# Performance work log

Hardware: AMD Instinct MI355X
Metric: run time of the kernel (lower is better)

Reference implementation:

```python
import jax, jax.numpy as jnp
import numpy as np

EPS = 1e-7  # tf.keras.backend.epsilon()
DEGREE = 5
SCALE_BASE = 1.0
SCALE_LEGENDRE = 1.0


def legendre_basis(x, degree):
    # min/max normalization over the feature axis -> x_norm in [-1, 1]
    x_min = jnp.min(x, axis=-1, keepdims=True)
    x_max = jnp.max(x, axis=-1, keepdims=True)
    x_norm = 2.0 * (x - x_min) / (x_max - x_min + EPS) - 1.0
    polys = [jnp.ones_like(x_norm), x_norm]
    for n in range(2, degree + 1):
        p_n = ((2 * n - 1) * x_norm * polys[-1] - (n - 1) * polys[-2]) / n
        polys.append(p_n)
    return jnp.stack(polys, axis=-1)  # [b, i, degree+1]


def setup_inputs() -> dict:
    key = jax.random.key(0)
    k1, k2, k3 = jax.random.split(key, 3)
    b, i, o, d = 4096, 1024, 1024, DEGREE + 1
    x = jax.random.normal(k1, (b, i), dtype=jnp.float32)
    # HeUniform: limit = sqrt(6 / fan_in)
    lim_b = np.sqrt(6.0 / i)
    base_weight = jax.random.uniform(k2, (i, o), dtype=jnp.float32, minval=-lim_b, maxval=lim_b)
    legendre_weight = jax.random.uniform(k3, (i, o, d), dtype=jnp.float32, minval=-lim_b, maxval=lim_b)
    return {"x": x, "base_weight": base_weight, "legendre_weight": legendre_weight}


def reference(x, base_weight, legendre_weight):
    base_output = jax.nn.silu(x @ base_weight)  # [b, o]
    basis = legendre_basis(x, DEGREE)  # [b, i, d]
    # 'bi,iod,bid->bo' == fold x into the basis then contract (i, d)
    xb = x[..., None] * basis  # [b, i, d]
    legendre_output = jnp.einsum('bid,iod->bo', xb, legendre_weight)
    return SCALE_BASE * base_output + SCALE_LEGENDRE * legendre_output
```

## Files before the change

### kernel.cpp

```cpp
#include <hip/hip_runtime.h>
#include <stdint.h>

typedef unsigned short u16;
typedef unsigned int   u32;
typedef __attribute__((ext_vector_type(8)))  short bhalf8;
typedef __attribute__((ext_vector_type(16))) float f32x16;

#define B_ROWS 4096
#define I_DIM  1024
#define O_DIM  1024
#define N_D    6
#define K_LEG  (I_DIM * N_D)

#define BM 256
#define BN 256
#define BK 32
#define NU 56
#define SLOT_BYTES 32768
#define LDS_BYTES  131072

__device__ __forceinline__ u16 f2b(float f) {
  u32 u = __float_as_uint(f);
  return (u16)((u + 0x7fffu + ((u >> 16) & 1u)) >> 16);
}
__device__ __forceinline__ float b2f(u16 h) {
  return __uint_as_float((u32)h << 16);
}

__device__ __forceinline__ void gld_lds16(const void* g, void* l) {
  __builtin_amdgcn_global_load_lds(
      (const __attribute__((address_space(1))) u32*)(uintptr_t)g,
      (__attribute__((address_space(3))) u32*)(u32)(uintptr_t)l, 16, 0, 0);
}

#define RS 201
__global__ void k_prep(const float* __restrict__ bw, const float* __restrict__ lw,
                       const float* __restrict__ x,
                       u16* __restrict__ Bb, u16* __restrict__ Bl,
                       u16* __restrict__ Ab, u16* __restrict__ Al) {
  __shared__ float t[32 * RS];
  if (blockIdx.x < 1024) {
    const int bx = blockIdx.x & 31, by = blockIdx.x >> 5;
    const int i0 = by * 32, o0 = bx * 32;
    const int c = threadIdx.x & 31, r0 = threadIdx.x >> 5;
    #pragma unroll
    for (int k = 0; k < 4; ++k) {
      int r = r0 + k * 8;
      t[r * 33 + c] = bw[(size_t)(i0 + r) * O_DIM + o0 + c];
    }
    __syncthreads();
    #pragma unroll
    for (int k = 0; k < 4; ++k) {
      int r = r0 + k * 8;
      Bb[(size_t)(o0 + r) * I_DIM + i0 + c] = f2b(t[c * 33 + r]);
    }
  } else if (blockIdx.x < 2048) {
    const int blk = blockIdx.x - 1024;
    const int bx = blk & 31, by = blk >> 5;
    const int i0 = by * 32, o0 = bx * 32;
    for (int q = threadIdx.x; q < 32 * 48; q += 256) {
      int ri = q / 48, s4 = q % 48;
      float4 v = *(const float4*)(lw + (size_t)(i0 + ri) * (O_DIM * N_D) + o0 * N_D + s4 * 4);
      float* p = t + ri * RS + s4 * 4;
      p[0] = v.x; p[1] = v.y; p[2] = v.z; p[3] = v.w;
    }
    __syncthreads();
    for (int q = threadIdx.x; q < 32 * 96; q += 256) {
      int ro = q / 96, k = q % 96;
      int e0 = 2 * k, e1 = 2 * k + 1;
      float v0 = t[(e0 / 6) * RS + ro * 6 + (e0 % 6)];
      float v1 = t[(e1 / 6) * RS + ro * 6 + (e1 % 6)];
      u32* dst = (u32*)(Bl + (size_t)(o0 + ro) * K_LEG + i0 * N_D);
      dst[k] = (u32)f2b(v0) | ((u32)f2b(v1) << 16);
    }
  } else {
    const int b = blockIdx.x - 2048;
    const int tt = threadIdx.x;
    float4 v = ((const float4*)(x + (size_t)b * I_DIM))[tt];
    float mn = fminf(fminf(v.x, v.y), fminf(v.z, v.w));
    float mx = fmaxf(fmaxf(v.x, v.y), fmaxf(v.z, v.w));
    #pragma unroll
    for (int off = 32; off > 0; off >>= 1) {
      mn = fminf(mn, __shfl_xor(mn, off, 64));
      mx = fmaxf(mx, __shfl_xor(mx, off, 64));
    }
    __shared__ float smn[4], smx[4];
    if ((tt & 63) == 0) { smn[tt >> 6] = mn; smx[tt >> 6] = mx; }
    __syncthreads();
    mn = fminf(fminf(smn[0], smn[1]), fminf(smn[2], smn[3]));
    mx = fmaxf(fmaxf(smx[0], smx[1]), fmaxf(smx[2], smx[3]));
    float sc = 2.0f / (mx - mn + 1e-7f);

    float xs[4] = {v.x, v.y, v.z, v.w};
    u32 lb[12];
    #pragma unroll
    for (int e = 0; e < 4; ++e) {
      float xv = xs[e];
      float xn = (xv - mn) * sc - 1.0f;
      float p0 = 1.0f, p1 = xn;
      float p2 = (3.0f * xn * p1 - 1.0f * p0) * (1.0f / 2.0f);
      float p3 = (5.0f * xn * p2 - 2.0f * p1) * (1.0f / 3.0f);
      float p4 = (7.0f * xn * p3 - 3.0f * p2) * (1.0f / 4.0f);
      float p5 = (9.0f * xn * p4 - 4.0f * p3) * (1.0f / 5.0f);
      lb[e * 3 + 0] = (u32)f2b(xv * p0) | ((u32)f2b(xv * p1) << 16);
      lb[e * 3 + 1] = (u32)f2b(xv * p2) | ((u32)f2b(xv * p3) << 16);
      lb[e * 3 + 2] = (u32)f2b(xv * p4) | ((u32)f2b(xv * p5) << 16);
    }
    u32 a0 = (u32)f2b(xs[0]) | ((u32)f2b(xs[1]) << 16);
    u32 a1 = (u32)f2b(xs[2]) | ((u32)f2b(xs[3]) << 16);
    *(uint2*)(Ab + (size_t)b * I_DIM + tt * 4) = make_uint2(a0, a1);
    uint4* dl = (uint4*)(Al + (size_t)b * K_LEG + tt * 24);
    dl[0] = make_uint4(lb[0], lb[1], lb[2], lb[3]);
    dl[1] = make_uint4(lb[4], lb[5], lb[6], lb[7]);
    dl[2] = make_uint4(lb[8], lb[9], lb[10], lb[11]);
  }
}

__global__ __launch_bounds__(512, 2) void k_gemm(
    const u16* __restrict__ Ab, const u16* __restrict__ Bb,
    const u16* __restrict__ Al, const u16* __restrict__ Bl,
    float* __restrict__ out, u16* __restrict__ Pb) {
  extern __shared__ char lds[];

  const int tid  = threadIdx.x;
  const int wave = tid >> 6;
  const int lane = tid & 63;
  const int wm = wave >> 2;
  const int wn = wave & 3;
  const u32 lr = (u32)lane & 31;
  const u32 hi = (u32)lane >> 5;

  const int bid   = blockIdx.x;
  const int bx    = bid >> 4;
  const int by    = (bid >> 2) & 3;
  const int split = bid & 3;
  const size_t brow = (size_t)bx * BM;
  const size_t bcol = (size_t)by * BN;
  const bool s0 = (split == 0);
  const int legbase = s0 ? 0 : (24 + 56 * (split - 1));

  const int r4 = tid >> 2;
  const u32 skey = (((u32)r4 >> 1) & 3) ^ (((u32)r4 >> 3) & 3);
  const size_t cs = (size_t)(((u32)(tid & 3) ^ skey) * 8);
  char* const l0 = lds + (u32)wave * 1024;

  const u16 *gA0, *gA1, *gB0, *gB1;
  auto set_ptrs = [&](const u16* A, const u16* Bt, size_t ldk, size_t kt) {
    const size_t ko = kt * BK + cs;
    gA0 = A  + (brow + r4) * ldk + ko;
    gA1 = A  + (brow + 128 + r4) * ldk + ko;
    gB0 = Bt + (bcol + r4) * ldk + ko;
    gB1 = Bt + (bcol + 128 + r4) * ldk + ko;
  };
  if (s0) set_ptrs(Ab, Bb, I_DIM, 0);
  else    set_ptrs(Al, Bl, K_LEG, (size_t)legbase);

  auto stage = [&](int v) {
    if (s0 && v == 32) set_ptrs(Al, Bl, K_LEG, 0);
    char* d = l0 + (size_t)(v & 3) * SLOT_BYTES;
    gld_lds16(gA0, d);          gld_lds16(gA1, d + 8192);
    gld_lds16(gB0, d + 16384);  gld_lds16(gB1, d + 24576);
    gA0 += BK; gA1 += BK; gB0 += BK; gB1 += BK;
  };

  const u32 key = ((lr >> 1) & 3) ^ ((lr >> 3) & 3);
  const u32 c00 = ((0 + hi) ^ key) * 16;
  const u32 c10 = ((2 + hi) ^ key) * 16;
  const u32 abase_r = (u32)wm * 8192 + lr * 64;
  const u32 bbase_r = 16384u + ((u32)wn >> 1) * 8192 + ((u32)wn & 1) * 4096 + lr * 64;

  f32x16 acc[4][2] = {};
  bhalf8 a0[4], b0[2], a1[4], b1[2], a2[4], b2[2];

  auto silu = [&]() {
    #pragma unroll
    for (int m = 0; m < 4; ++m)
      #pragma unroll
      for (int n = 0; n < 2; ++n)
        #pragma unroll
        for (int j = 0; j < 16; ++j) {
          float v = acc[m][n][j];
          acc[m][n][j] = v / (1.0f + __expf(-v));
        }
  };

#define FILL(u1, CH, AA, BB) do {                                             \
    const char* pn_ = lds + (size_t)((u1) & 3) * SLOT_BYTES;                  \
    BB[0] = *(const bhalf8*)(pn_ + bbase_r + (CH));                           \
    BB[1] = *(const bhalf8*)(pn_ + bbase_r + 2048 + (CH));                    \
    AA[0] = *(const bhalf8*)(pn_ + abase_r + (CH));                           \
    AA[1] = *(const bhalf8*)(pn_ + abase_r + 2048 + (CH));                    \
    AA[2] = *(const bhalf8*)(pn_ + abase_r + 4096 + (CH));                    \
    AA[3] = *(const bhalf8*)(pn_ + abase_r + 6144 + (CH));                    \
  } while (0)

#define MM(AA, BB) do {                                                       \
    __builtin_amdgcn_sched_barrier(0);                                        \
    __builtin_amdgcn_s_setprio(1);                                            \
    _Pragma("unroll")                                                         \
    for (int m = 0; m < 4; ++m)                                               \
      _Pragma("unroll")                                                       \
      for (int n = 0; n < 2; ++n)                                             \
        acc[m][n] = __builtin_amdgcn_mfma_f32_32x32x16_bf16(AA[m], BB[n], acc[m][n], 0, 0, 0); \
    __builtin_amdgcn_s_setprio(0);                                            \
    __builtin_amdgcn_sched_barrier(0);                                        \
  } while (0)

#define TILE(u, PA, PB, QA, QB, RA, RB) do {                                  \
    const int u_ = (u);                                                       \
    if (s0 && u_ == 32) silu();                                               \
    if (u_ <= NU - 3) {                                                       \
      stage(u_ + 2);                                                          \
      asm volatile("s_waitcnt vmcnt(4)" ::: "memory");   \
    } else {                                                                  \
      asm volatile("s_waitcnt vmcnt(0)" ::: "memory");                        \
    }                                                                         \
    __builtin_amdgcn_s_barrier();                                             \
    if (u_ < NU - 1) FILL(u_ + 1, c00, RA, RB);                               \
    MM(PA, PB);                                                               \
    if (u_ < NU - 1) FILL(u_ + 1, c10, PA, PB);                               \
    MM(QA, QB);                                                               \
  } while (0)

  stage(0); stage(1);
  asm volatile("s_waitcnt vmcnt(4)" ::: "memory");
  __builtin_amdgcn_s_barrier();
  FILL(0, c00, a0, b0);
  FILL(0, c10, a1, b1);

  for (int t = 0; t < 18; ++t) {
    const int u = t * 3;
    TILE(u,     a0, b0, a1, b1, a2, b2);
    TILE(u + 1, a2, b2, a0, b0, a1, b1);
    TILE(u + 2, a1, b1, a2, b2, a0, b0);
  }
  TILE(54, a0, b0, a1, b1, a2, b2);
  TILE(55, a2, b2, a0, b0, a1, b1);
#undef TILE
#undef MM
#undef FILL

  if (s0) {
    #pragma unroll
    for (int m = 0; m < 4; ++m)
      #pragma unroll
      for (int n = 0; n < 2; ++n) {
        const size_t rb = brow + wm * 128 + m * 32 + 4 * hi;
        const size_t c  = bcol + wn * 64 + n * 32 + lr;
        #pragma unroll
        for (int j = 0; j < 16; ++j) {
          const size_t r = rb + (j & 3) + 8 * (j >> 2);
          out[r * O_DIM + c] = acc[m][n][j];
        }
      }
  } else {
    u16* dst = Pb + (size_t)(split - 1) * ((size_t)B_ROWS * O_DIM);
    #pragma unroll
    for (int m = 0; m < 4; ++m)
      #pragma unroll
      for (int n = 0; n < 2; ++n) {
        const size_t rb = brow + wm * 128 + m * 32 + 4 * hi;
        const size_t c  = bcol + wn * 64 + n * 32 + lr;
        #pragma unroll
        for (int j = 0; j < 16; ++j) {
          const size_t r = rb + (j & 3) + 8 * (j >> 2);
          dst[r * O_DIM + c] = f2b(acc[m][n][j]);
        }
      }
  }
}

__global__ void k_reduce(float* __restrict__ out, const u16* __restrict__ Pb) {
  const size_t i = (size_t)blockIdx.x * 256 + threadIdx.x;
  const size_t NE = (size_t)B_ROWS * O_DIM;
  float4 a = ((const float4*)out)[i];
  ushort4 p0 = ((const ushort4*)Pb)[i];
  ushort4 p1 = ((const ushort4*)(Pb + NE))[i];
  ushort4 p2 = ((const ushort4*)(Pb + 2 * NE))[i];
  a.x += b2f(p0.x) + b2f(p1.x) + b2f(p2.x);
  a.y += b2f(p0.y) + b2f(p1.y) + b2f(p2.y);
  a.z += b2f(p0.z) + b2f(p1.z) + b2f(p2.z);
  a.w += b2f(p0.w) + b2f(p1.w) + b2f(p2.w);
  ((float4*)out)[i] = a;
}

extern "C" void kernel_launch(void* const* d_in, const int* in_sizes, int n_in,
                              void* d_out, int out_size, void* d_ws, size_t ws_size,
                              hipStream_t stream) {
  const float* x  = (const float*)d_in[0];
  const float* bw = (const float*)d_in[1];
  const float* lw = (const float*)d_in[2];
  float* out = (float*)d_out;

  char* w = (char*)d_ws;
  u16* Ab = (u16*)(w);
  u16* Al = (u16*)(w + (size_t)8   * 1024 * 1024);
  u16* Bb = (u16*)(w + (size_t)56  * 1024 * 1024);
  u16* Bl = (u16*)(w + (size_t)58  * 1024 * 1024);
  u16* Pb = (u16*)(w + (size_t)72  * 1024 * 1024);

  hipFuncSetAttribute((const void*)k_gemm,
                      hipFuncAttributeMaxDynamicSharedMemorySize, LDS_BYTES);

  k_prep  <<<dim3(2048 + B_ROWS), 256, 0, stream>>>(bw, lw, x, Bb, Bl, Ab, Al);
  k_gemm  <<<dim3(256), 512, LDS_BYTES, stream>>>(Ab, Bb, Al, Bl, out, Pb);
  k_reduce<<<dim3((B_ROWS * O_DIM / 4) / 256), 256, 0, stream>>>(out, Pb);
}
```

Before: 104.3 us.

## Shrink GEMM tiles to 128x128 with 4 waves and 3-stage LDS buffering

Reduces the block tile from 256x256 with 8 waves to 128x128 with 4 waves, which raises the grid from 256 to 1024 blocks and targets three blocks per CU. The LDS pipeline becomes three 16KB slots with one-ahead staging. Register prefetch of the next tile's fragments is dropped in favour of reading the current slot right after the barrier. Smaller tiles lower arithmetic intensity and raise global and LDS traffic per FLOP. In exchange they give better CU occupancy and latency hiding through multiple resident blocks.

```diff
diff --git a/kernel.cpp b/kernel.cpp
--- a/kernel.cpp
+++ b/kernel.cpp
@@ -12,12 +12,12 @@
 #define N_D    6
 #define K_LEG  (I_DIM * N_D)
 
-#define BM 256
-#define BN 256
+#define BM 128
+#define BN 128
 #define BK 32
-#define NU 56
-#define SLOT_BYTES 32768
-#define LDS_BYTES  131072
+#define NS 56
+#define SLOT 16384
+#define LDS_BYTES 49152
 
 __device__ __forceinline__ u16 f2b(float f) {
   u32 u = __float_as_uint(f);
@@ -116,7 +116,7 @@
   }
 }
 
-__global__ __launch_bounds__(512, 2) void k_gemm(
+__global__ __launch_bounds__(256, 3) void k_gemm(
     const u16* __restrict__ Ab, const u16* __restrict__ Bb,
     const u16* __restrict__ Al, const u16* __restrict__ Bl,
     float* __restrict__ out, u16* __restrict__ Pb) {
@@ -125,15 +125,16 @@
   const int tid  = threadIdx.x;
   const int wave = tid >> 6;
   const int lane = tid & 63;
-  const int wm = wave >> 2;
-  const int wn = wave & 3;
+  const int wm = wave >> 1;
+  const int wn = wave & 1;
   const u32 lr = (u32)lane & 31;
   const u32 hi = (u32)lane >> 5;
 
   const int bid   = blockIdx.x;
-  const int bx    = bid >> 4;
-  const int by    = (bid >> 2) & 3;
-  const int split = bid & 3;
+  const int split = bid >> 8;
+  const int rem   = bid & 255;
+  const int by    = rem >> 5;
+  const int bx    = rem & 31;
   const size_t brow = (size_t)bx * BM;
   const size_t bcol = (size_t)by * BN;
   const bool s0 = (split == 0);
@@ -142,39 +143,39 @@
   const int r4 = tid >> 2;
   const u32 skey = (((u32)r4 >> 1) & 3) ^ (((u32)r4 >> 3) & 3);
   const size_t cs = (size_t)(((u32)(tid & 3) ^ skey) * 8);
-  char* const l0 = lds + (u32)wave * 1024;
 
   const u16 *gA0, *gA1, *gB0, *gB1;
   auto set_ptrs = [&](const u16* A, const u16* Bt, size_t ldk, size_t kt) {
     const size_t ko = kt * BK + cs;
     gA0 = A  + (brow + r4) * ldk + ko;
-    gA1 = A  + (brow + 128 + r4) * ldk + ko;
+    gA1 = A  + (brow + 64 + r4) * ldk + ko;
     gB0 = Bt + (bcol + r4) * ldk + ko;
-    gB1 = Bt + (bcol + 128 + r4) * ldk + ko;
+    gB1 = Bt + (bcol + 64 + r4) * ldk + ko;
   };
   if (s0) set_ptrs(Ab, Bb, I_DIM, 0);
   else    set_ptrs(Al, Bl, K_LEG, (size_t)legbase);
 
-  auto stage = [&](int v) {
+  auto stage = [&](int v, char* sb) {
     if (s0 && v == 32) set_ptrs(Al, Bl, K_LEG, 0);
-    char* d = l0 + (size_t)(v & 3) * SLOT_BYTES;
-    gld_lds16(gA0, d);          gld_lds16(gA1, d + 8192);
-    gld_lds16(gB0, d + 16384);  gld_lds16(gB1, d + 24576);
+    gld_lds16(gA0, sb + (size_t)tid * 16);
+    gld_lds16(gA1, sb + 4096 + (size_t)tid * 16);
+    gld_lds16(gB0, sb + 8192 + (size_t)tid * 16);
+    gld_lds16(gB1, sb + 12288 + (size_t)tid * 16);
     gA0 += BK; gA1 += BK; gB0 += BK; gB1 += BK;
   };
 
   const u32 key = ((lr >> 1) & 3) ^ ((lr >> 3) & 3);
   const u32 c00 = ((0 + hi) ^ key) * 16;
   const u32 c10 = ((2 + hi) ^ key) * 16;
-  const u32 abase_r = (u32)wm * 8192 + lr * 64;
-  const u32 bbase_r = 16384u + ((u32)wn >> 1) * 8192 + ((u32)wn & 1) * 4096 + lr * 64;
-
-  f32x16 acc[4][2] = {};
-  bhalf8 a0[4], b0[2], a1[4], b1[2], a2[4], b2[2];
+  const u32 abase = ((u32)wm * 64 + lr) * 64;
+  const u32 bbase = 8192u + ((u32)wn * 64 + lr) * 64;
+
+  f32x16 acc[2][2] = {};
+  bhalf8 a0[2], b0[2], a1[2], b1[2];
 
   auto silu = [&]() {
     #pragma unroll
-    for (int m = 0; m < 4; ++m)
+    for (int m = 0; m < 2; ++m)
       #pragma unroll
       for (int n = 0; n < 2; ++n)
         #pragma unroll
@@ -184,21 +185,18 @@
         }
   };
 
-#define FILL(u1, CH, AA, BB) do {                                             \
-    const char* pn_ = lds + (size_t)((u1) & 3) * SLOT_BYTES;                  \
-    BB[0] = *(const bhalf8*)(pn_ + bbase_r + (CH));                           \
-    BB[1] = *(const bhalf8*)(pn_ + bbase_r + 2048 + (CH));                    \
-    AA[0] = *(const bhalf8*)(pn_ + abase_r + (CH));                           \
-    AA[1] = *(const bhalf8*)(pn_ + abase_r + 2048 + (CH));                    \
-    AA[2] = *(const bhalf8*)(pn_ + abase_r + 4096 + (CH));                    \
-    AA[3] = *(const bhalf8*)(pn_ + abase_r + 6144 + (CH));                    \
+#define RD(AA, BB, SB_, CH) do {                                              \
+    BB[0] = *(const bhalf8*)((SB_) + bbase + (CH));                           \
+    BB[1] = *(const bhalf8*)((SB_) + bbase + 2048 + (CH));                    \
+    AA[0] = *(const bhalf8*)((SB_) + abase + (CH));                           \
+    AA[1] = *(const bhalf8*)((SB_) + abase + 2048 + (CH));                    \
   } while (0)
 
 #define MM(AA, BB) do {                                                       \
     __builtin_amdgcn_sched_barrier(0);                                        \
     __builtin_amdgcn_s_setprio(1);                                            \
     _Pragma("unroll")                                                         \
-    for (int m = 0; m < 4; ++m)                                               \
+    for (int m = 0; m < 2; ++m)                                               \
       _Pragma("unroll")                                                       \
       for (int n = 0; n < 2; ++n)                                             \
         acc[m][n] = __builtin_amdgcn_mfma_f32_32x32x16_bf16(AA[m], BB[n], acc[m][n], 0, 0, 0); \
@@ -206,46 +204,44 @@
     __builtin_amdgcn_sched_barrier(0);                                        \
   } while (0)
 
-#define TILE(u, PA, PB, QA, QB, RA, RB) do {                                  \
+#define TILE(u, CUR, NXT, DOSTG, WTN) do {                                    \
     const int u_ = (u);                                                       \
     if (s0 && u_ == 32) silu();                                               \
-    if (u_ <= NU - 3) {                                                       \
-      stage(u_ + 2);                                                          \
-      asm volatile("s_waitcnt vmcnt(4)" ::: "memory");   \
-    } else {                                                                  \
-      asm volatile("s_waitcnt vmcnt(0)" ::: "memory");                        \
-    }                                                                         \
+    if (DOSTG) stage(u_ + 1, (NXT));                                          \
+    asm volatile("s_waitcnt vmcnt(" #WTN ")" ::: "memory");                   \
     __builtin_amdgcn_s_barrier();                                             \
-    if (u_ < NU - 1) FILL(u_ + 1, c00, RA, RB);                               \
-    MM(PA, PB);                                                               \
-    if (u_ < NU - 1) FILL(u_ + 1, c10, PA, PB);                               \
-    MM(QA, QB);                                                               \
+    RD(a0, b0, (CUR), c00);                                                   \
+    RD(a1, b1, (CUR), c10);                                                   \
+    MM(a0, b0);                                                               \
+    MM(a1, b1);                                                               \
   } while (0)
 
-  stage(0); stage(1);
-  asm volatile("s_waitcnt vmcnt(4)" ::: "memory");
+  char* const s_0 = lds;
+  char* const s_1 = lds + SLOT;
+  char* const s_2 = lds + 2 * SLOT;
+
+  stage(0, s_0);
+  asm volatile("s_waitcnt vmcnt(0)" ::: "memory");
   __builtin_amdgcn_s_barrier();
-  FILL(0, c00, a0, b0);
-  FILL(0, c10, a1, b1);
 
   for (int t = 0; t < 18; ++t) {
     const int u = t * 3;
-    TILE(u,     a0, b0, a1, b1, a2, b2);
-    TILE(u + 1, a2, b2, a0, b0, a1, b1);
-    TILE(u + 2, a1, b1, a2, b2, a0, b0);
+    TILE(u,     s_0, s_1, true, 4);
+    TILE(u + 1, s_1, s_2, true, 4);
+    TILE(u + 2, s_2, s_0, true, 4);
   }
-  TILE(54, a0, b0, a1, b1, a2, b2);
-  TILE(55, a2, b2, a0, b0, a1, b1);
+  TILE(54, s_0, s_1, true, 4);
+  TILE(55, s_1, s_2, false, 0);
 #undef TILE
 #undef MM
-#undef FILL
+#undef RD
 
   if (s0) {
     #pragma unroll
-    for (int m = 0; m < 4; ++m)
+    for (int m = 0; m < 2; ++m)
       #pragma unroll
       for (int n = 0; n < 2; ++n) {
-        const size_t rb = brow + wm * 128 + m * 32 + 4 * hi;
+        const size_t rb = brow + wm * 64 + m * 32 + 4 * hi;
         const size_t c  = bcol + wn * 64 + n * 32 + lr;
         #pragma unroll
         for (int j = 0; j < 16; ++j) {
@@ -256,10 +252,10 @@
   } else {
     u16* dst = Pb + (size_t)(split - 1) * ((size_t)B_ROWS * O_DIM);
     #pragma unroll
-    for (int m = 0; m < 4; ++m)
+    for (int m = 0; m < 2; ++m)
       #pragma unroll
       for (int n = 0; n < 2; ++n) {
-        const size_t rb = brow + wm * 128 + m * 32 + 4 * hi;
+        const size_t rb = brow + wm * 64 + m * 32 + 4 * hi;
         const size_t c  = bcol + wn * 64 + n * 32 + lr;
         #pragma unroll
         for (int j = 0; j < 16; ++j) {
@@ -303,6 +299,6 @@
                       hipFuncAttributeMaxDynamicSharedMemorySize, LDS_BYTES);
 
   k_prep  <<<dim3(2048 + B_ROWS), 256, 0, stream>>>(bw, lw, x, Bb, Bl, Ab, Al);
-  k_gemm  <<<dim3(256), 512, LDS_BYTES, stream>>>(Ab, Bb, Al, Bl, out, Pb);
+  k_gemm  <<<dim3(4 * (B_ROWS / BM) * (O_DIM / BN)), 256, LDS_BYTES, stream>>>(Ab, Bb, Al, Bl, out, Pb);
   k_reduce<<<dim3((B_ROWS * O_DIM / 4) / 256), 256, 0, stream>>>(out, Pb);
 }
```

New measurement: 113.8 us. 1.09x slower.
